# Performance work log

Measured on AMD Instinct MI355X. Metric: run time of the kernel, lower is better.

Reference implementation:

```python
import jax, jax.numpy as jnp
import numpy as np

BATCH, FEAT = 128, 1024
CLS = 500
HID = 512

def setup_inputs() -> dict:
    key = jax.random.key(0)
    ks = jax.random.split(key, 6)
    return {
        "image_feats": jax.random.normal(ks[0], (BATCH, FEAT), dtype=jnp.float32),
        "attributes": jax.random.normal(ks[1], (CLS, FEAT), dtype=jnp.float32),
        "W1": jax.random.normal(ks[2], (HID, 2 * FEAT), dtype=jnp.float32) * 0.02,
        "b1": jax.random.normal(ks[3], (HID,), dtype=jnp.float32) * 0.02,
        "W2": jax.random.normal(ks[4], (1, HID), dtype=jnp.float32) * 0.02,
        "b2": jax.random.normal(ks[5], (1,), dtype=jnp.float32) * 0.02,
    }

def reference(image_feats, attributes, W1, b1, W2, b2):
    feat_dim = image_feats.shape[1]
    # fc1 on cat([img, attr]) == img @ W1[:, :F].T + attr @ W1[:, F:].T + b1
    # computed via broadcast-add, never materializing the (B, C, 2F) concat.
    img_part = image_feats @ W1[:, :feat_dim].T          # (B, HID)
    attr_part = attributes @ W1[:, feat_dim:].T          # (C, HID)
    h = jax.nn.relu(img_part[:, None, :] + attr_part[None, :, :] + b1)  # (B, C, HID)
    out = jax.nn.sigmoid(jnp.einsum('bch,oh->bco', h, W2) + b2)          # (B, C, 1)
    return out[..., 0]  # (B, C)
```

## Files before the change

kernel.cpp:

```cpp
#include <hip/hip_runtime.h>
#include <math.h>

#define BATCH 128
#define FEAT  1024
#define CLS   500
#define HID   512
#define SPL   8

constexpr int BM = 64, BN = 64, BK = 16;

__global__ __launch_bounds__(256) void gemm_bt_splitk(
    const float* __restrict__ img, const float* __restrict__ attr,
    const float* __restrict__ W1,
    float* __restrict__ imgP, float* __restrict__ attrP)
{
    __shared__ float As[BK][BM + 4];
    __shared__ float Bs[BK][BN + 4];

    const int t  = threadIdx.x;
    const int z  = blockIdx.z;
    const int n0 = blockIdx.x * BN;

    const float* A;
    float* P;
    int M, boff, m0;
    if (blockIdx.y < 2) {
        A = img;  P = imgP;  M = BATCH; boff = 0;
        m0 = blockIdx.y * BM;
    } else {
        A = attr; P = attrP; M = CLS;  boff = FEAT;
        m0 = (blockIdx.y - 2) * BM;
    }

    const int K    = FEAT;
    const int ldb  = 2 * FEAT;
    const int Ks   = K / SPL;
    const int kb   = z * Ks;

    const int lrow = t >> 2;
    const int lk4  = (t & 3) * 4;

    const int tn = t & 15;
    const int tm = t >> 4;

    const bool aok = (m0 + lrow) < M;
    const float* Arow = A  + (size_t)(m0 + lrow) * K;
    const float* Brow = W1 + (size_t)(n0 + lrow) * ldb + boff;

    float4 av = aok ? *(const float4*)&Arow[kb + lk4]
                    : make_float4(0.f, 0.f, 0.f, 0.f);
    float4 bv = *(const float4*)&Brow[kb + lk4];

    float acc[4][4];
    #pragma unroll
    for (int i = 0; i < 4; ++i)
        #pragma unroll
        for (int j = 0; j < 4; ++j) acc[i][j] = 0.f;

    for (int kt = 0; kt < Ks; kt += BK) {
        As[lk4 + 0][lrow] = av.x;
        As[lk4 + 1][lrow] = av.y;
        As[lk4 + 2][lrow] = av.z;
        As[lk4 + 3][lrow] = av.w;
        Bs[lk4 + 0][lrow] = bv.x;
        Bs[lk4 + 1][lrow] = bv.y;
        Bs[lk4 + 2][lrow] = bv.z;
        Bs[lk4 + 3][lrow] = bv.w;
        __syncthreads();

        if (kt + BK < Ks) {
            av = aok ? *(const float4*)&Arow[kb + kt + BK + lk4]
                     : make_float4(0.f, 0.f, 0.f, 0.f);
            bv = *(const float4*)&Brow[kb + kt + BK + lk4];
        }

        #pragma unroll
        for (int k = 0; k < BK; ++k) {
            const float4 a = *(const float4*)&As[k][tm * 4];
            const float4 b = *(const float4*)&Bs[k][tn * 4];
            acc[0][0] = fmaf(a.x, b.x, acc[0][0]);
            acc[0][1] = fmaf(a.x, b.y, acc[0][1]);
            acc[0][2] = fmaf(a.x, b.z, acc[0][2]);
            acc[0][3] = fmaf(a.x, b.w, acc[0][3]);
            acc[1][0] = fmaf(a.y, b.x, acc[1][0]);
            acc[1][1] = fmaf(a.y, b.y, acc[1][1]);
            acc[1][2] = fmaf(a.y, b.z, acc[1][2]);
            acc[1][3] = fmaf(a.y, b.w, acc[1][3]);
            acc[2][0] = fmaf(a.z, b.x, acc[2][0]);
            acc[2][1] = fmaf(a.z, b.y, acc[2][1]);
            acc[2][2] = fmaf(a.z, b.z, acc[2][2]);
            acc[2][3] = fmaf(a.z, b.w, acc[2][3]);
            acc[3][0] = fmaf(a.w, b.x, acc[3][0]);
            acc[3][1] = fmaf(a.w, b.y, acc[3][1]);
            acc[3][2] = fmaf(a.w, b.z, acc[3][2]);
            acc[3][3] = fmaf(a.w, b.w, acc[3][3]);
        }
        __syncthreads();
    }

    float* Pz = P + (size_t)z * M * HID;
    #pragma unroll
    for (int i = 0; i < 4; ++i) {
        const int m = m0 + tm * 4 + i;
        if (m < M) {
            float4 v = make_float4(acc[i][0], acc[i][1], acc[i][2], acc[i][3]);
            *(float4*)&Pz[(size_t)m * HID + n0 + tn * 4] = v;
        }
    }
}

__global__ __launch_bounds__(256) void merge_kernel(
    const float* __restrict__ imgP, const float* __restrict__ attrP,
    const float* __restrict__ b1,
    float* __restrict__ imgF, float* __restrict__ attrF)
{
    const int NIMG  = BATCH * HID;
    const int NATTR = CLS * HID;
    const int idx = blockIdx.x * 256 + threadIdx.x;
    if (idx < NIMG) {
        float s = 0.f;
        #pragma unroll
        for (int zz = 0; zz < SPL; ++zz) s += imgP[zz * NIMG + idx];
        imgF[idx] = s + b1[idx & (HID - 1)];
    } else if (idx < NIMG + NATTR) {
        const int j = idx - NIMG;
        float s = 0.f;
        #pragma unroll
        for (int zz = 0; zz < SPL; ++zz) s += attrP[zz * NATTR + j];
        attrF[j] = s;
    }
}

constexpr int PC = 64;
constexpr int HC = 128;

__global__ __launch_bounds__(256) void pair_kernel(
    const float* __restrict__ imgF, const float* __restrict__ attrF,
    const float* __restrict__ W2, const float* __restrict__ b2,
    float* __restrict__ out)
{
    __shared__ float4 V[(HC / 4) * PC];

    const int t   = threadIdx.x;
    const int ci  = t & 63;
    const int wid = __builtin_amdgcn_readfirstlane(t >> 6);
    const int b   = blockIdx.y * 4 + wid;
    const int c0  = blockIdx.x * PC;

    const float* up = imgF + (size_t)b * HID;

    float ax = 0.f, ay = 0.f, az = 0.f, aw = 0.f;

    for (int hc = 0; hc < HID; hc += HC) {
        __syncthreads();
        #pragma unroll
        for (int rep = 0; rep < 8; ++rep) {
            const int idx = rep * 256 + t;
            const int r   = idx >> 5;
            const int f4  = idx & 31;
            float4 v = make_float4(0.f, 0.f, 0.f, 0.f);
            if (c0 + r < CLS)
                v = *(const float4*)&attrF[(size_t)(c0 + r) * HID + hc + f4 * 4];
            V[f4 * PC + ((r ^ f4) & 63)] = v;
        }
        __syncthreads();

        #pragma unroll
        for (int h4 = 0; h4 < HC / 4; ++h4) {
            const float4 v = V[h4 * PC + ((ci ^ h4) & 63)];
            const float4 u = *(const float4*)&up[hc + h4 * 4];
            const float4 w = *(const float4*)&W2[hc + h4 * 4];
            ax = fmaf(fmaxf(u.x + v.x, 0.f), w.x, ax);
            ay = fmaf(fmaxf(u.y + v.y, 0.f), w.y, ay);
            az = fmaf(fmaxf(u.z + v.z, 0.f), w.z, az);
            aw = fmaf(fmaxf(u.w + v.w, 0.f), w.w, aw);
        }
    }

    const int c = c0 + ci;
    if (c < CLS) {
        const float x = (ax + ay) + (az + aw) + b2[0];
        out[(size_t)b * CLS + c] = 1.f / (1.f + __expf(-x));
    }
}

extern "C" void kernel_launch(void* const* d_in, const int* in_sizes, int n_in,
                              void* d_out, int out_size, void* d_ws, size_t ws_size,
                              hipStream_t stream) {
    const float* img  = (const float*)d_in[0];
    const float* attr = (const float*)d_in[1];
    const float* W1   = (const float*)d_in[2];
    const float* b1   = (const float*)d_in[3];
    const float* W2   = (const float*)d_in[4];
    const float* b2   = (const float*)d_in[5];
    float* out = (float*)d_out;

    float* ws    = (float*)d_ws;
    float* imgP  = ws;
    float* attrP = imgP  + (size_t)SPL * BATCH * HID;
    float* imgF  = attrP + (size_t)SPL * CLS * HID;
    float* attrF = imgF  + (size_t)BATCH * HID;

    dim3 ggrid(HID / BN, 2 + 8, SPL);
    gemm_bt_splitk<<<ggrid, 256, 0, stream>>>(img, attr, W1, imgP, attrP);

    const int ntot = BATCH * HID + CLS * HID;
    merge_kernel<<<(ntot + 255) / 256, 256, 0, stream>>>(imgP, attrP, b1, imgF, attrF);

    dim3 pgrid((CLS + PC - 1) / PC, BATCH / 4);
    pair_kernel<<<pgrid, 256, 0, stream>>>(imgF, attrF, W2, b2, out);
}
```

Before: 110.2 us.

## Use bf16 MFMA for the split-K projection GEMM

Replaces the FP32 FMA outer-product GEMM with a version that converts A and W1 tiles to bf16 (round-half-up bit packing) in shared memory and uses 16x16x32 bf16 MFMA instructions, one wave per 16-row slab. BK is doubled to 32, so each split-K chunk takes 4 iterations. This cuts scalar FMA work in the projection stage. It lowers the precision of the fc1 products, and the output stores become scalar per element instead of float4.

```diff
diff --git a/kernel.cpp b/kernel.cpp
--- a/kernel.cpp
+++ b/kernel.cpp
@@ -7,15 +7,25 @@
 #define HID   512
 #define SPL   8
 
-constexpr int BM = 64, BN = 64, BK = 16;
-
-__global__ __launch_bounds__(256) void gemm_bt_splitk(
+typedef short s16x8 __attribute__((ext_vector_type(8)));
+typedef float f32x4 __attribute__((ext_vector_type(4)));
+
+__device__ inline unsigned pkbf(float x, float y) {
+    unsigned ux = __float_as_uint(x) + 0x8000u;
+    unsigned uy = __float_as_uint(y) + 0x8000u;
+    return __builtin_amdgcn_perm(uy, ux, 0x07060302u);
+}
+
+constexpr int BM = 64, BN = 64, BK = 32;
+constexpr int LDA = BK + 8;
+
+__global__ __launch_bounds__(256) void gemm_bt_mfma(
     const float* __restrict__ img, const float* __restrict__ attr,
     const float* __restrict__ W1,
     float* __restrict__ imgP, float* __restrict__ attrP)
 {
-    __shared__ float As[BK][BM + 4];
-    __shared__ float Bs[BK][BN + 4];
+    __shared__ unsigned short As[BM * LDA];
+    __shared__ unsigned short Bs[BN * LDA];
 
     const int t  = threadIdx.x;
     const int z  = blockIdx.z;
@@ -32,79 +42,70 @@
         m0 = (blockIdx.y - 2) * BM;
     }
 
-    const int K    = FEAT;
-    const int ldb  = 2 * FEAT;
-    const int Ks   = K / SPL;
-    const int kb   = z * Ks;
-
-    const int lrow = t >> 2;
-    const int lk4  = (t & 3) * 4;
-
-    const int tn = t & 15;
-    const int tm = t >> 4;
-
-    const bool aok = (m0 + lrow) < M;
-    const float* Arow = A  + (size_t)(m0 + lrow) * K;
-    const float* Brow = W1 + (size_t)(n0 + lrow) * ldb + boff;
-
-    float4 av = aok ? *(const float4*)&Arow[kb + lk4]
-                    : make_float4(0.f, 0.f, 0.f, 0.f);
-    float4 bv = *(const float4*)&Brow[kb + lk4];
-
-    float acc[4][4];
+    const int K   = FEAT;
+    const int ldb = 2 * FEAT;
+    const int Ks  = K / SPL;
+    const int kb  = z * Ks;
+
+    const int srow = t >> 2;
+    const int skq  = (t & 3) * 8;
+
+    const bool aok = (m0 + srow) < M;
+    const float* Arow = A  + (size_t)(m0 + srow) * K  + kb;
+    const float* Brow = W1 + (size_t)(n0 + srow) * ldb + boff + kb;
+
+    const int lane = t & 63;
+    const int wid  = t >> 6;
+    const int ln   = lane & 15;
+    const int quad = lane >> 4;
+
+    f32x4 acc[4];
     #pragma unroll
-    for (int i = 0; i < 4; ++i)
-        #pragma unroll
-        for (int j = 0; j < 4; ++j) acc[i][j] = 0.f;
-
-    for (int kt = 0; kt < Ks; kt += BK) {
-        As[lk4 + 0][lrow] = av.x;
-        As[lk4 + 1][lrow] = av.y;
-        As[lk4 + 2][lrow] = av.z;
-        As[lk4 + 3][lrow] = av.w;
-        Bs[lk4 + 0][lrow] = bv.x;
-        Bs[lk4 + 1][lrow] = bv.y;
-        Bs[lk4 + 2][lrow] = bv.z;
-        Bs[lk4 + 3][lrow] = bv.w;
-        __syncthreads();
-
-        if (kt + BK < Ks) {
-            av = aok ? *(const float4*)&Arow[kb + kt + BK + lk4]
-                     : make_float4(0.f, 0.f, 0.f, 0.f);
-            bv = *(const float4*)&Brow[kb + kt + BK + lk4];
-        }
-
-        #pragma unroll
-        for (int k = 0; k < BK; ++k) {
-            const float4 a = *(const float4*)&As[k][tm * 4];
-            const float4 b = *(const float4*)&Bs[k][tn * 4];
-            acc[0][0] = fmaf(a.x, b.x, acc[0][0]);
-            acc[0][1] = fmaf(a.x, b.y, acc[0][1]);
-            acc[0][2] = fmaf(a.x, b.z, acc[0][2]);
-            acc[0][3] = fmaf(a.x, b.w, acc[0][3]);
-            acc[1][0] = fmaf(a.y, b.x, acc[1][0]);
-            acc[1][1] = fmaf(a.y, b.y, acc[1][1]);
-            acc[1][2] = fmaf(a.y, b.z, acc[1][2]);
-            acc[1][3] = fmaf(a.y, b.w, acc[1][3]);
-            acc[2][0] = fmaf(a.z, b.x, acc[2][0]);
-            acc[2][1] = fmaf(a.z, b.y, acc[2][1]);
-            acc[2][2] = fmaf(a.z, b.z, acc[2][2]);
-            acc[2][3] = fmaf(a.z, b.w, acc[2][3]);
-            acc[3][0] = fmaf(a.w, b.x, acc[3][0]);
-            acc[3][1] = fmaf(a.w, b.y, acc[3][1]);
-            acc[3][2] = fmaf(a.w, b.z, acc[3][2]);
-            acc[3][3] = fmaf(a.w, b.w, acc[3][3]);
+    for (int nt = 0; nt < 4; ++nt) acc[nt] = (f32x4){0.f, 0.f, 0.f, 0.f};
+
+    float4 a0, a1, b0, b1;
+    a0 = aok ? *(const float4*)&Arow[skq]     : make_float4(0.f, 0.f, 0.f, 0.f);
+    a1 = aok ? *(const float4*)&Arow[skq + 4] : make_float4(0.f, 0.f, 0.f, 0.f);
+    b0 = *(const float4*)&Brow[skq];
+    b1 = *(const float4*)&Brow[skq + 4];
+
+    #pragma unroll
+    for (int c = 0; c < 4; ++c) {
+        {
+            uint4 pa = make_uint4(pkbf(a0.x, a0.y), pkbf(a0.z, a0.w),
+                                  pkbf(a1.x, a1.y), pkbf(a1.z, a1.w));
+            uint4 pb = make_uint4(pkbf(b0.x, b0.y), pkbf(b0.z, b0.w),
+                                  pkbf(b1.x, b1.y), pkbf(b1.z, b1.w));
+            *(uint4*)&As[srow * LDA + skq] = pa;
+            *(uint4*)&Bs[srow * LDA + skq] = pb;
+        }
+        __syncthreads();
+
+        if (c < 3) {
+            const int ko = (c + 1) * BK + skq;
+            a0 = aok ? *(const float4*)&Arow[ko]     : make_float4(0.f, 0.f, 0.f, 0.f);
+            a1 = aok ? *(const float4*)&Arow[ko + 4] : make_float4(0.f, 0.f, 0.f, 0.f);
+            b0 = *(const float4*)&Brow[ko];
+            b1 = *(const float4*)&Brow[ko + 4];
+        }
+
+        const s16x8 af = *(const s16x8*)&As[(wid * 16 + ln) * LDA + quad * 8];
+        #pragma unroll
+        for (int nt = 0; nt < 4; ++nt) {
+            const s16x8 bf = *(const s16x8*)&Bs[(nt * 16 + ln) * LDA + quad * 8];
+            acc[nt] = __builtin_amdgcn_mfma_f32_16x16x32_bf16(af, bf, acc[nt], 0, 0, 0);
         }
         __syncthreads();
     }
 
     float* Pz = P + (size_t)z * M * HID;
     #pragma unroll
-    for (int i = 0; i < 4; ++i) {
-        const int m = m0 + tm * 4 + i;
-        if (m < M) {
-            float4 v = make_float4(acc[i][0], acc[i][1], acc[i][2], acc[i][3]);
-            *(float4*)&Pz[(size_t)m * HID + n0 + tn * 4] = v;
+    for (int nt = 0; nt < 4; ++nt) {
+        #pragma unroll
+        for (int r = 0; r < 4; ++r) {
+            const int m = m0 + wid * 16 + quad * 4 + r;
+            if (m < M)
+                Pz[(size_t)m * HID + n0 + nt * 16 + ln] = acc[nt][r];
         }
     }
 }
@@ -202,7 +203,7 @@
     float* attrF = imgF  + (size_t)BATCH * HID;
 
     dim3 ggrid(HID / BN, 2 + 8, SPL);
-    gemm_bt_splitk<<<ggrid, 256, 0, stream>>>(img, attr, W1, imgP, attrP);
+    gemm_bt_mfma<<<ggrid, 256, 0, stream>>>(img, attr, W1, imgP, attrP);
 
     const int ntot = BATCH * HID + CLS * HID;
     merge_kernel<<<(ntot + 255) / 256, 256, 0, stream>>>(imgP, attrP, b1, imgF, attrF);
```

New measurement: 104.2 us. -5.4%, faster.
